# Kernel optimization log

Hardware: AMD Instinct MI355X
Metric: run time of the kernel (lower is better)

The kernel has to match this reference:

```python
import jax, jax.numpy as jnp
import numpy as np
from jax import lax


def binarize(x):
    # tf.sign with 0 mapped to +1
    return jnp.where(x >= 0, jnp.ones_like(x), -jnp.ones_like(x))


def setup_inputs() -> dict:
    key = jax.random.key(0)
    kx, kw = jax.random.split(key)
    x = jax.random.normal(kx, (64, 56, 56, 128), dtype=jnp.float32)
    # weights init: normal stddev=0.1, shape (kh, kw, in_ch, filters) == HWIO
    w = jax.random.normal(kw, (3, 3, 128, 256), dtype=jnp.float32) * 0.1
    return {"x": x, "w": w}


def reference(x, w):
    x_bin = binarize(x)
    w_bin = binarize(w)
    # NHWC input, HWIO kernel, SAME padding, stride (1,1)
    out = lax.conv_general_dilated(
        x_bin, w_bin,
        window_strides=(1, 1),
        padding="SAME",
        dimension_numbers=("NHWC", "HWIO", "NHWC"),
    )
    return out
```

## Files before the change

kernel.cpp:

```cpp
#include <hip/hip_runtime.h>
#include <stdint.h>


#define IH 56
#define IW 56
#define COUT 256
#define NB 64
#define ROWPX 58
#define PXB 144
#define ROWB (ROWPX * PXB)

typedef int v4i  __attribute__((ext_vector_type(4)));
typedef int v16i __attribute__((ext_vector_type(16)));

__device__ __forceinline__ uint32_t nib(uint64_t w, int i) {
    return ((uint32_t)(w >> (4 * i)) & 0xF) * 0x00204081u & 0x01010101u;
}

__global__ void pack_x_kernel(const float* __restrict__ x,
                              uint64_t* __restrict__ xp, int npix) {
    int gtid = blockIdx.x * blockDim.x + threadIdx.x;
    int wave = gtid >> 6, lane = gtid & 63;
    int nw = (gridDim.x * blockDim.x) >> 6;
    const float2* x2 = (const float2*)x;
    int q = npix >> 2;
    for (int p = wave; p < q; p += nw) {
        float2 v0 = x2[(size_t)p * 64 + lane];
        float2 v1 = x2[((size_t)p + q) * 64 + lane];
        float2 v2 = x2[((size_t)p + 2 * q) * 64 + lane];
        float2 v3 = x2[((size_t)p + 3 * q) * 64 + lane];
        uint64_t a0 = __ballot(v0.x < 0.0f), a1 = __ballot(v0.y < 0.0f);
        uint64_t b0 = __ballot(v1.x < 0.0f), b1 = __ballot(v1.y < 0.0f);
        uint64_t c0 = __ballot(v2.x < 0.0f), c1 = __ballot(v2.y < 0.0f);
        uint64_t d0 = __ballot(v3.x < 0.0f), d1 = __ballot(v3.y < 0.0f);
        if (lane == 0) {
            xp[2 * (size_t)p] = a0;             xp[2 * (size_t)p + 1] = a1;
            xp[2 * ((size_t)p + q)] = b0;       xp[2 * ((size_t)p + q) + 1] = b1;
            xp[2 * ((size_t)p + 2 * q)] = c0;   xp[2 * ((size_t)p + 2 * q) + 1] = c1;
            xp[2 * ((size_t)p + 3 * q)] = d0;   xp[2 * ((size_t)p + 3 * q) + 1] = d1;
        }
    }
}

__global__ void pack_w_kernel(const float* __restrict__ w,
                              uint64_t* __restrict__ wp) {
    int gtid = blockIdx.x * blockDim.x + threadIdx.x;
    int wave = gtid >> 6, lane = gtid & 63;
    int nw = (gridDim.x * blockDim.x) >> 6;
    const int ntask = 9 * 2 * COUT;
    for (int t = wave; t < ntask; t += nw) {
        int oc = t & 255, hf = (t >> 8) & 1, tap = t >> 9;
        float v = w[((size_t)(tap * 128 + 2 * lane + hf)) * COUT + oc];
        uint64_t m = __ballot(v < 0.0f);
        if (lane == 0) wp[(size_t)(tap * 2 + hf) * COUT + oc] = m;
    }
}

__global__ void swz_w_kernel(const uint64_t* __restrict__ wp,
                             char* __restrict__ bsw, int* __restrict__ kct) {
    int t = blockIdx.x * blockDim.x + threadIdx.x;
    if (t < 36 * 8 * 64) {
        int lane = t & 63, ntks = t >> 6;
        int nt = ntks & 7, ks = ntks >> 3;
        int oc = nt * 32 + (lane & 31);
        int kk = ks * 32 + (lane >> 5) * 16;
        int tap = kk >> 7, c = kk & 127;
        int hf = c >> 6, bit0 = c & 63;
        uint64_t word = wp[(size_t)(tap * 2 + hf) * COUT + oc];
        int4 d;
        d.x = (int)nib(word, (bit0 >> 2) + 0);
        d.y = (int)nib(word, (bit0 >> 2) + 1);
        d.z = (int)nib(word, (bit0 >> 2) + 2);
        d.w = (int)nib(word, (bit0 >> 2) + 3);
        *(int4*)(bsw + (size_t)t * 16) = d;
    } else if (t < 36 * 8 * 64 + 256) {
        int oc = t - 36 * 8 * 64;
        int Sw[9];
#pragma unroll
        for (int tp = 0; tp < 9; ++tp)
            Sw[tp] = __popcll(wp[(size_t)(tp * 2) * COUT + oc]) +
                     __popcll(wp[(size_t)(tp * 2 + 1) * COUT + oc]);
        for (int hc = 0; hc < 3; ++hc)
            for (int wc = 0; wc < 3; ++wc) {
                int K = 0;
                for (int kh = 0; kh < 3; ++kh) {
                    if (hc == 0 && kh == 0) continue;
                    if (hc == 2 && kh == 2) continue;
                    for (int kw = 0; kw < 3; ++kw) {
                        if (wc == 0 && kw == 0) continue;
                        if (wc == 2 && kw == 2) continue;
                        K += 128 - 2 * Sw[kh * 3 + kw];
                    }
                }
                kct[(hc * 3 + wc) * COUT + oc] = K;
            }
    }
}

__global__ __launch_bounds__(256, 2) void bconv_mfma(
        const uint64_t* __restrict__ xp,
        const char* __restrict__ bsw,
        const int* __restrict__ kct,
        float* __restrict__ out) {
    __shared__ alignas(16) char xs8[4 * ROWB];
    __shared__ int pc[4][ROWPX];
    __shared__ int sx9[2][IW];

    int bh = blockIdx.x % 28, n = blockIdx.x / 28;
    int hbase = bh * 2;
    int tid = threadIdx.x;

    for (int t = tid; t < 4 * ROWPX; t += 256) {
        int row = t / ROWPX, col = t % ROWPX;
        int rr = hbase - 1 + row, cc = col - 1;
        uint64_t w0 = 0, w1 = 0;
        if ((unsigned)rr < IH && (unsigned)cc < IW) {
            const uint64_t* pp = xp + 2 * (((size_t)n * IH + rr) * IW + cc);
            w0 = pp[0]; w1 = pp[1];
        }
        pc[row][col] = __popcll(w0) + __popcll(w1);
        int4* dst4 = (int4*)(xs8 + row * ROWB + col * PXB);
#pragma unroll
        for (int gi = 0; gi < 4; ++gi) {
            int4 d;
            d.x = (int)nib(w0, 4 * gi + 0);
            d.y = (int)nib(w0, 4 * gi + 1);
            d.z = (int)nib(w0, 4 * gi + 2);
            d.w = (int)nib(w0, 4 * gi + 3);
            dst4[gi] = d;
        }
#pragma unroll
        for (int gi = 0; gi < 4; ++gi) {
            int4 d;
            d.x = (int)nib(w1, 4 * gi + 0);
            d.y = (int)nib(w1, 4 * gi + 1);
            d.z = (int)nib(w1, 4 * gi + 2);
            d.w = (int)nib(w1, 4 * gi + 3);
            dst4[4 + gi] = d;
        }
    }
    __syncthreads();

    for (int t = tid; t < 2 * IW; t += 256) {
        int g = t / IW, px = t % IW;
        int s = 0;
#pragma unroll
        for (int kh = 0; kh < 3; ++kh)
            s += pc[g + kh][px] + pc[g + kh][px + 1] + pc[g + kh][px + 2];
        sx9[g][px] = s;
    }
    __syncthreads();

    int wv = tid >> 6, lane = tid & 63;
    int g = wv >> 1;
    int nt0 = (wv & 1) * 4;
    int m = lane & 31, half = lane >> 5;

    v16i acc[2][4];
#pragma unroll
    for (int mt = 0; mt < 2; ++mt)
#pragma unroll
        for (int j = 0; j < 4; ++j)
#pragma unroll
            for (int r = 0; r < 16; ++r) acc[mt][j][r] = 0;

    const v4i* bbase = (const v4i*)bsw + (size_t)nt0 * 64 + lane;
    const char* abase = xs8 + g * ROWB + half * 16 + m * PXB;

    v4i b0[4], b1[4], b2[4];

#define LB(buf, ks)                                              \
    do {                                                         \
        const v4i* _p = bbase + (size_t)(ks) * 512;              \
        buf[0] = _p[0];   buf[1] = _p[64];                       \
        buf[2] = _p[128]; buf[3] = _p[192];                      \
    } while (0)

#define STEPK(ks, buf)                                           \
    do {                                                         \
        int _tap = (ks) >> 2, _kc = (ks) & 3;                    \
        const char* _ar = abase + (_tap / 3) * ROWB +            \
                          (_tap % 3) * PXB + _kc * 32;           \
        v4i _a0 = *(const v4i*)(_ar);                            \
        v4i _a1 = *(const v4i*)(_ar + 24 * PXB);                 \
        _Pragma("unroll")                                        \
        for (int _j = 0; _j < 4; ++_j) {                         \
            acc[0][_j] = __builtin_amdgcn_mfma_i32_32x32x32_i8(  \
                _a0, buf[_j], acc[0][_j], 0, 0, 0);              \
            acc[1][_j] = __builtin_amdgcn_mfma_i32_32x32x32_i8(  \
                _a1, buf[_j], acc[1][_j], 0, 0, 0);              \
        }                                                        \
    } while (0)

    LB(b0, 0);
    LB(b1, 1);
    for (int ks = 0; ks < 36; ks += 3) {
        LB(b2, ks + 2);
        STEPK(ks, b0);
        LB(b0, (ks + 3 < 36) ? ks + 3 : 0);
        STEPK(ks + 1, b1);
        LB(b1, (ks + 4 < 36) ? ks + 4 : 0);
        STEPK(ks + 2, b2);
    }

    int h = hbase + g;
    int hc = (h == 0) ? 0 : ((h == IH - 1) ? 2 : 1);
    float* orow = out + (((size_t)n * IH + h) * IW) * COUT;

    int sxv[2][16];
#pragma unroll
    for (int r = 0; r < 16; ++r) {
        int pxr = (r & 3) + 8 * (r >> 2) + 4 * half;
        sxv[0][r] = sx9[g][pxr];
        sxv[1][r] = sx9[g][24 + pxr];
    }

#pragma unroll
    for (int j = 0; j < 4; ++j) {
        int ocj = (nt0 + j) * 32 + m;
        int Ki  = kct[(hc * 3 + 1) * COUT + ocj];
        int K0  = kct[(hc * 3 + 0) * COUT + ocj];
        int K55 = kct[(hc * 3 + 2) * COUT + ocj];
#pragma unroll
        for (int mt = 0; mt < 2; ++mt) {
            int Mb = mt ? 24 : 0;
#pragma unroll
            for (int r = 0; r < 16; ++r) {
                int pxr = (r & 3) + 8 * (r >> 2) + 4 * half;
                int px = Mb + pxr;
                int K = Ki;
                if (mt == 0 && r == 0 && half == 0) K = K0;
                if (mt == 1 && r == 15 && half == 1) K = K55;
                float o = (float)(K - 2 * sxv[mt][r] + 4 * acc[mt][j][r]);
                orow[(size_t)px * COUT + ocj] = o;
            }
        }
    }
}

extern "C" void kernel_launch(void* const* d_in, const int* in_sizes, int n_in,
                              void* d_out, int out_size, void* d_ws, size_t ws_size,
                              hipStream_t stream) {
    const float* x = (const float*)d_in[0];
    const float* w = (const float*)d_in[1];
    float* out = (float*)d_out;

    uint64_t* wp  = (uint64_t*)d_ws;
    int*      kct = (int*)((char*)d_ws + 36864);
    char*     bsw = (char*)d_ws + 46080;
    uint64_t* xp  = (uint64_t*)((char*)d_ws + 344064);

    const int npix = NB * IH * IW;

    pack_x_kernel<<<6272, 256, 0, stream>>>(x, xp, npix);
    pack_w_kernel<<<288, 256, 0, stream>>>(w, wp);
    swz_w_kernel<<<73, 256, 0, stream>>>(wp, bsw, kct);
    bconv_mfma<<<NB * 28, 256, 0, stream>>>(xp, bsw, kct, out);
}
```

Baseline: 364.4 us.

## Use 8 waves per block, one output-channel tile each, with MFMA priority

The block grows from 256 to 512 threads. Each wave now owns a single 32-channel output tile and covers both output rows, so each wave loads one B fragment per k-step instead of four. Accumulators drop from 8 to 4 v16i per wave, which lowers register pressure and allows higher occupancy (launch_bounds 512,4). The wave also adds s_setprio around its MFMA bursts and fully unrolls the k loop. In exchange, each wave reads four A fragments from LDS per step, so A traffic per MFMA goes up, and the B global loads are no longer amortised across multiple tiles.

```diff
diff --git a/kernel.cpp b/kernel.cpp
--- a/kernel.cpp
+++ b/kernel.cpp
@@ -97,7 +97,7 @@
     }
 }
 
-__global__ __launch_bounds__(256, 2) void bconv_mfma(
+__global__ __launch_bounds__(512, 4) void bconv_mfma(
         const uint64_t* __restrict__ xp,
         const char* __restrict__ bsw,
         const int* __restrict__ kct,
@@ -110,7 +110,7 @@
     int hbase = bh * 2;
     int tid = threadIdx.x;
 
-    for (int t = tid; t < 4 * ROWPX; t += 256) {
+    for (int t = tid; t < 4 * ROWPX; t += 512) {
         int row = t / ROWPX, col = t % ROWPX;
         int rr = hbase - 1 + row, cc = col - 1;
         uint64_t w0 = 0, w1 = 0;
@@ -141,7 +141,7 @@
     }
     __syncthreads();
 
-    for (int t = tid; t < 2 * IW; t += 256) {
+    for (int t = tid; t < 2 * IW; t += 512) {
         int g = t / IW, px = t % IW;
         int s = 0;
 #pragma unroll
@@ -152,28 +152,23 @@
     __syncthreads();
 
     int wv = tid >> 6, lane = tid & 63;
-    int g = wv >> 1;
-    int nt0 = (wv & 1) * 4;
+    int nt = wv;
     int m = lane & 31, half = lane >> 5;
 
-    v16i acc[2][4];
-#pragma unroll
-    for (int mt = 0; mt < 2; ++mt)
-#pragma unroll
-        for (int j = 0; j < 4; ++j)
-#pragma unroll
-            for (int r = 0; r < 16; ++r) acc[mt][j][r] = 0;
-
-    const v4i* bbase = (const v4i*)bsw + (size_t)nt0 * 64 + lane;
-    const char* abase = xs8 + g * ROWB + half * 16 + m * PXB;
-
-    v4i b0[4], b1[4], b2[4];
+    v16i acc[4];
+#pragma unroll
+    for (int a = 0; a < 4; ++a)
+#pragma unroll
+        for (int r = 0; r < 16; ++r) acc[a][r] = 0;
+
+    const v4i* bbase = (const v4i*)bsw + (size_t)nt * 64 + lane;
+    const char* abase = xs8 + half * 16 + m * PXB;
+
+    v4i b0, b1, b2;
 
 #define LB(buf, ks)                                              \
     do {                                                         \
-        const v4i* _p = bbase + (size_t)(ks) * 512;              \
-        buf[0] = _p[0];   buf[1] = _p[64];                       \
-        buf[2] = _p[128]; buf[3] = _p[192];                      \
+        buf = bbase[(size_t)(ks) * 512];                         \
     } while (0)
 
 #define STEPK(ks, buf)                                           \
@@ -181,19 +176,25 @@
         int _tap = (ks) >> 2, _kc = (ks) & 3;                    \
         const char* _ar = abase + (_tap / 3) * ROWB +            \
                           (_tap % 3) * PXB + _kc * 32;           \
-        v4i _a0 = *(const v4i*)(_ar);                            \
-        v4i _a1 = *(const v4i*)(_ar + 24 * PXB);                 \
-        _Pragma("unroll")                                        \
-        for (int _j = 0; _j < 4; ++_j) {                         \
-            acc[0][_j] = __builtin_amdgcn_mfma_i32_32x32x32_i8(  \
-                _a0, buf[_j], acc[0][_j], 0, 0, 0);              \
-            acc[1][_j] = __builtin_amdgcn_mfma_i32_32x32x32_i8(  \
-                _a1, buf[_j], acc[1][_j], 0, 0, 0);              \
-        }                                                        \
+        v4i _a00 = *(const v4i*)(_ar);                           \
+        v4i _a01 = *(const v4i*)(_ar + 24 * PXB);                \
+        v4i _a10 = *(const v4i*)(_ar + ROWB);                    \
+        v4i _a11 = *(const v4i*)(_ar + ROWB + 24 * PXB);         \
+        __builtin_amdgcn_s_setprio(1);                           \
+        acc[0] = __builtin_amdgcn_mfma_i32_32x32x32_i8(          \
+            _a00, buf, acc[0], 0, 0, 0);                         \
+        acc[1] = __builtin_amdgcn_mfma_i32_32x32x32_i8(          \
+            _a01, buf, acc[1], 0, 0, 0);                         \
+        acc[2] = __builtin_amdgcn_mfma_i32_32x32x32_i8(          \
+            _a10, buf, acc[2], 0, 0, 0);                         \
+        acc[3] = __builtin_amdgcn_mfma_i32_32x32x32_i8(          \
+            _a11, buf, acc[3], 0, 0, 0);                         \
+        __builtin_amdgcn_s_setprio(0);                           \
     } while (0)
 
     LB(b0, 0);
     LB(b1, 1);
+#pragma unroll
     for (int ks = 0; ks < 36; ks += 3) {
         LB(b2, ks + 2);
         STEPK(ks, b0);
@@ -203,24 +204,15 @@
         STEPK(ks + 2, b2);
     }
 
-    int h = hbase + g;
-    int hc = (h == 0) ? 0 : ((h == IH - 1) ? 2 : 1);
-    float* orow = out + (((size_t)n * IH + h) * IW) * COUT;
-
-    int sxv[2][16];
-#pragma unroll
-    for (int r = 0; r < 16; ++r) {
-        int pxr = (r & 3) + 8 * (r >> 2) + 4 * half;
-        sxv[0][r] = sx9[g][pxr];
-        sxv[1][r] = sx9[g][24 + pxr];
-    }
-
-#pragma unroll
-    for (int j = 0; j < 4; ++j) {
-        int ocj = (nt0 + j) * 32 + m;
-        int Ki  = kct[(hc * 3 + 1) * COUT + ocj];
-        int K0  = kct[(hc * 3 + 0) * COUT + ocj];
-        int K55 = kct[(hc * 3 + 2) * COUT + ocj];
+    int oc = nt * 32 + m;
+#pragma unroll
+    for (int g = 0; g < 2; ++g) {
+        int h = hbase + g;
+        int hc = (h == 0) ? 0 : ((h == IH - 1) ? 2 : 1);
+        float* orow = out + (((size_t)n * IH + h) * IW) * COUT;
+        int Ki  = kct[(hc * 3 + 1) * COUT + oc];
+        int K0  = kct[(hc * 3 + 0) * COUT + oc];
+        int K55 = kct[(hc * 3 + 2) * COUT + oc];
 #pragma unroll
         for (int mt = 0; mt < 2; ++mt) {
             int Mb = mt ? 24 : 0;
@@ -231,8 +223,8 @@
                 int K = Ki;
                 if (mt == 0 && r == 0 && half == 0) K = K0;
                 if (mt == 1 && r == 15 && half == 1) K = K55;
-                float o = (float)(K - 2 * sxv[mt][r] + 4 * acc[mt][j][r]);
-                orow[(size_t)px * COUT + ocj] = o;
+                float o = (float)(K - 2 * sx9[g][px] + 4 * acc[g * 2 + mt][r]);
+                orow[(size_t)px * COUT + oc] = o;
             }
         }
     }
@@ -255,5 +247,5 @@
     pack_x_kernel<<<6272, 256, 0, stream>>>(x, xp, npix);
     pack_w_kernel<<<288, 256, 0, stream>>>(w, wp);
     swz_w_kernel<<<73, 256, 0, stream>>>(wp, bsw, kct);
-    bconv_mfma<<<NB * 28, 256, 0, stream>>>(xp, bsw, kct, out);
-}
+    bconv_mfma<<<NB * 28, 512, 0, stream>>>(xp, bsw, kct, out);
+}
```

Result: faster. 316.8 us (-13.1%).
